# Performance work log

Measured on AMD Instinct MI355X. Metric: run time of the kernel, lower is better.

Reference implementation:

```python
import jax, jax.numpy as jnp
import numpy as np
import itertools

B, N, IN_DIM, H_DIM, OUT_DIM, K = 64, 32, 128, 512, 256, 2


def _uniform(key, shape, fan_in):
    bound = 1.0 / np.sqrt(fan_in)
    return jax.random.uniform(key, shape, jnp.float32, -bound, bound)


def setup_inputs() -> dict:
    key = jax.random.key(0)
    ks = jax.random.split(key, 7)
    x = jax.random.normal(ks[0], (B, N, IN_DIM), jnp.float32)
    W1 = _uniform(ks[1], (IN_DIM * K, H_DIM), IN_DIM * K)
    b1 = _uniform(ks[2], (H_DIM,), IN_DIM * K)
    W2 = _uniform(ks[3], (H_DIM, H_DIM), H_DIM)
    b2 = _uniform(ks[4], (H_DIM,), H_DIM)
    W3 = _uniform(ks[5], (H_DIM, OUT_DIM), H_DIM)
    b3 = _uniform(ks[6], (OUT_DIM,), H_DIM)
    return {"x": x, "W1": W1, "b1": b1, "W2": W2, "b2": b2, "W3": W3, "b3": b3}


def reference(x, W1, b1, W2, b2, W3, b3):
    n = x.shape[1]
    # all k-permutations of set indices, itertools order: [P, K], P = N*(N-1) for K=2
    perm = jnp.asarray(np.array(list(itertools.permutations(range(n), K)), dtype=np.int32))
    # gather: [B, P, K, in_dim] -> flatten last two dims -> [B, P, K*in_dim]
    xp = x[:, perm, :].reshape(x.shape[0], perm.shape[0], K * x.shape[2])
    h = jax.nn.relu(jnp.einsum('bpf,fh->bph', xp, W1) + b1)
    h = jax.nn.relu(jnp.einsum('bph,hg->bpg', h, W2) + b2)
    out = jnp.einsum('bpg,go->bpo', h, W3) + b3
    return out.sum(axis=1)  # sum over permutations -> [B, out_dim]
```

## Files before the change

### kernel.cpp

```cpp
#include <hip/hip_runtime.h>

#define BB 64
#define NN 32
#define IND 128
#define HD 512
#define OD 256
#define NPERM 992

typedef __attribute__((ext_vector_type(8))) _Float16 half8;
typedef __attribute__((ext_vector_type(4))) _Float16 half4;
typedef __attribute__((ext_vector_type(16))) float f32x16;

typedef __attribute__((address_space(3))) char lds_char_t;
typedef __attribute__((address_space(1))) const char gbl_char_t;

__device__ __forceinline__ void glds16(const void* g, void* l) {
    __builtin_amdgcn_global_load_lds((gbl_char_t*)g, (lds_char_t*)l, 16, 0, 0);
}

#define WAITVM6 asm volatile("s_waitcnt vmcnt(6)" ::: "memory")
#define WAITVM2 asm volatile("s_waitcnt vmcnt(2)" ::: "memory")
#define WAITVM1 asm volatile("s_waitcnt vmcnt(1)" ::: "memory")
#define WAITLGKM asm volatile("s_waitcnt lgkmcnt(0)" ::: "memory")
#define RBAR __builtin_amdgcn_s_barrier()

__device__ __forceinline__ half8 relu8(half8 x) {
    half8 z = 0;
    return __builtin_elementwise_max(x, z);
}

#define XTO 69632
__global__ __launch_bounds__(512, 4) void kprep(
    const float* __restrict__ x, const float* __restrict__ W1, const float* __restrict__ b1,
    const float* __restrict__ W2, _Float16* __restrict__ W2t,
    const float* __restrict__ b3, float* __restrict__ out,
    _Float16* __restrict__ U, _Float16* __restrict__ Vo) {
    __shared__ char smem[(256 + 32) * 272];
    const int bid = blockIdx.x;
    const int t = threadIdx.x;

    if (bid >= 256) {
        const int bid2 = bid - 256;
        float (*tile)[65] = (float (*)[65])smem;
        if (t < 256) out[(size_t)bid2 * OD + t] = (float)NPERM * b3[t];
        const int k0 = (bid2 & 7) * 64, c0 = (bid2 >> 3) * 64;
        const int cin = t & 63, r0 = (t >> 6) * 8;
#pragma unroll
        for (int rr = 0; rr < 8; ++rr)
            tile[r0 + rr][cin] = W2[(size_t)(k0 + r0 + rr) * HD + c0 + cin];
        __syncthreads();
        const int kout = t & 63;
#pragma unroll
        for (int rr = 0; rr < 8; ++rr) {
            int c = r0 + rr;
            W2t[(size_t)(c0 + c) * HD + k0 + kout] = (_Float16)tile[kout][c];
        }
        return;
    }

    const int g = bid & 3, b = bid >> 2;
    const int h0 = (g & 1) * 256;
    const int koff = (g >> 1) * 128;

    {
        const int n = t >> 4, c8 = (t & 15) * 8;
        const float* src = x + ((size_t)(b * NN + n)) * IND + c8;
        float4 f0 = *(const float4*)src;
        float4 f1 = *(const float4*)(src + 4);
        half8 h;
        h[0] = (_Float16)f0.x; h[1] = (_Float16)f0.y;
        h[2] = (_Float16)f0.z; h[3] = (_Float16)f0.w;
        h[4] = (_Float16)f1.x; h[5] = (_Float16)f1.y;
        h[6] = (_Float16)f1.z; h[7] = (_Float16)f1.w;
        *(half8*)(smem + XTO + n * 272 + c8 * 2) = h;
    }
    {
        const int ht = t & 63, ktb = t >> 6;
#pragma unroll
        for (int it = 0; it < 4; ++it) {
            const int kt = ktb + it * 8;
            const float* wsrc = W1 + (size_t)(koff + kt * 4) * HD + h0 + ht * 4;
            float4 v0 = *(const float4*)(wsrc);
            float4 v1 = *(const float4*)(wsrc + HD);
            float4 v2 = *(const float4*)(wsrc + 2 * HD);
            float4 v3 = *(const float4*)(wsrc + 3 * HD);
            char* wdst = smem + (size_t)(ht * 4) * 272 + kt * 8;
            half4 o0 = {(_Float16)v0.x, (_Float16)v1.x, (_Float16)v2.x, (_Float16)v3.x};
            half4 o1 = {(_Float16)v0.y, (_Float16)v1.y, (_Float16)v2.y, (_Float16)v3.y};
            half4 o2 = {(_Float16)v0.z, (_Float16)v1.z, (_Float16)v2.z, (_Float16)v3.z};
            half4 o3 = {(_Float16)v0.w, (_Float16)v1.w, (_Float16)v2.w, (_Float16)v3.w};
            *(half4*)(wdst) = o0;
            *(half4*)(wdst + 272) = o1;
            *(half4*)(wdst + 544) = o2;
            *(half4*)(wdst + 816) = o3;
        }
    }
    __syncthreads();

    const int lane = t & 63, wv = t >> 6;
    const int l31 = lane & 31, hi = lane >> 5;
    const char* abase = smem + XTO + (size_t)l31 * 272 + hi * 16;
    const char* bbase = smem + (size_t)(wv * 32 + l31) * 272 + hi * 16;

    f32x16 acc;
#pragma unroll
    for (int r = 0; r < 16; ++r) acc[r] = 0.f;
#pragma unroll
    for (int ks = 0; ks < 8; ++ks) {
        half8 a  = *(const half8*)(abase + ks * 32);
        half8 bf = *(const half8*)(bbase + ks * 32);
        acc = __builtin_amdgcn_mfma_f32_32x32x16_f16(a, bf, acc, 0, 0, 0);
    }
    const int hglob = h0 + wv * 32 + l31;
    const float bias = (g < 2) ? b1[hglob] : 0.f;
    _Float16* dst = ((g < 2) ? U : Vo) + (size_t)b * NN * HD + hglob;
#pragma unroll
    for (int r = 0; r < 16; ++r) {
        int row = (r & 3) + 8 * (r >> 2) + 4 * hi;
        dst[(size_t)row * HD] = (_Float16)(acc[r] + bias);
    }
}

#define SLOT0 65536
#define SLOT1 81920
__global__ __launch_bounds__(512, 2) void k2(
    const _Float16* __restrict__ Ug, const _Float16* __restrict__ Vg,
    const _Float16* __restrict__ W2t, const float* __restrict__ b2,
    const float* __restrict__ W3, float* __restrict__ out) {
    __shared__ char smb[98304];
    __shared__ float red[8][64];
    __shared__ float hred[64];

    const int bp = blockIdx.x;
    const int cb0 = blockIdx.y * 64;
    const int t = threadIdx.x;
    const int lane = t & 63, wid = t >> 6;
    const int l31 = lane & 31, hi = lane >> 5;
    const int lh = lane >> 5, lm = lane & 31;
    const unsigned sw = (unsigned)((l31 & 15) << 4);

    auto issueB = [&](int kh) {
#pragma unroll
        for (int ii = 0; ii < 4; ++ii) {
            int r = wid * 8 + ii * 2 + lh;
            const char* src = (const char*)W2t + (size_t)(cb0 + r) * 1024 + kh * 512
                              + ((lm * 16) ^ ((r & 15) << 4));
            glds16(src, smb + kh * 32768 + (wid * 8 + ii * 2) * 512);
        }
    };
    auto issueV = [&](int bb, int kh, unsigned slotOff) {
#pragma unroll
        for (int ii = 0; ii < 2; ++ii) {
            int r = wid * 4 + ii * 2 + lh;
            const char* src = (const char*)Vg + (size_t)(bb * NN + r) * 1024 + kh * 512
                              + ((lm * 16) ^ ((r & 15) << 4));
            glds16(src, smb + slotOff + (wid * 4 + ii * 2) * 512);
        }
    };

    const int bA = bp * 2, bB = bp * 2 + 1;
    issueB(0);
    issueV(bA, 0, SLOT0);
    issueB(1);
    issueV(bA, 1, SLOT1);
    WAITVM6;
    RBAR;

    f32x16 acc[4][2];
    auto resetAcc = [&]() {
#pragma unroll
        for (int rf = 0; rf < 4; ++rf)
#pragma unroll
            for (int cf = 0; cf < 2; ++cf)
#pragma unroll
                for (int r = 0; r < 16; ++r) acc[rf][cf][r] = 0.f;
    };

    auto compute = [&](int bb, int kh, unsigned slotOff) {
        const char* ubase = (const char*)Ug + (size_t)(bb * NN + wid * 4) * 1024
                            + kh * 512 + hi * 16;
        const unsigned vb = slotOff + (unsigned)(l31 * 512);
        const unsigned bb0 = (unsigned)(kh * 32768 + l31 * 512);
        const unsigned bb1 = (unsigned)(kh * 32768 + (32 + l31) * 512);

        half8 pU0, pU1, pU2, pU3, pV, pB0, pB1;
        {
            unsigned kx = ((unsigned)(hi * 16)) ^ sw;
            pU0 = *(const half8*)(ubase + 0 * 1024);
            pU1 = *(const half8*)(ubase + 1 * 1024);
            pU2 = *(const half8*)(ubase + 2 * 1024);
            pU3 = *(const half8*)(ubase + 3 * 1024);
            pV  = *(const half8*)(smb + vb + kx);
            pB0 = *(const half8*)(smb + bb0 + kx);
            pB1 = *(const half8*)(smb + bb1 + kx);
        }
#pragma unroll
        for (int kk = 0; kk < 16; ++kk) {
            half8 cU0 = pU0, cU1 = pU1, cU2 = pU2, cU3 = pU3;
            half8 cV = pV, cB0 = pB0, cB1 = pB1;
            if (kk < 15) {
                int kn = kk + 1;
                unsigned kx = ((unsigned)(kn * 32 + hi * 16)) ^ sw;
                pU0 = *(const half8*)(ubase + 0 * 1024 + kn * 32);
                pU1 = *(const half8*)(ubase + 1 * 1024 + kn * 32);
                pU2 = *(const half8*)(ubase + 2 * 1024 + kn * 32);
                pU3 = *(const half8*)(ubase + 3 * 1024 + kn * 32);
                pV  = *(const half8*)(smb + vb + kx);
                pB0 = *(const half8*)(smb + bb0 + kx);
                pB1 = *(const half8*)(smb + bb1 + kx);
            }

            __builtin_amdgcn_s_setprio(1);
            half8 af0 = relu8(cU0 + cV);
            acc[0][0] = __builtin_amdgcn_mfma_f32_32x32x16_f16(af0, cB0, acc[0][0], 0, 0, 0);
            acc[0][1] = __builtin_amdgcn_mfma_f32_32x32x16_f16(af0, cB1, acc[0][1], 0, 0, 0);
            half8 af1 = relu8(cU1 + cV);
            acc[1][0] = __builtin_amdgcn_mfma_f32_32x32x16_f16(af1, cB0, acc[1][0], 0, 0, 0);
            acc[1][1] = __builtin_amdgcn_mfma_f32_32x32x16_f16(af1, cB1, acc[1][1], 0, 0, 0);
            half8 af2 = relu8(cU2 + cV);
            acc[2][0] = __builtin_amdgcn_mfma_f32_32x32x16_f16(af2, cB0, acc[2][0], 0, 0, 0);
            acc[2][1] = __builtin_amdgcn_mfma_f32_32x32x16_f16(af2, cB1, acc[2][1], 0, 0, 0);
            half8 af3 = relu8(cU3 + cV);
            acc[3][0] = __builtin_amdgcn_mfma_f32_32x32x16_f16(af3, cB0, acc[3][0], 0, 0, 0);
            acc[3][1] = __builtin_amdgcn_mfma_f32_32x32x16_f16(af3, cB1, acc[3][1], 0, 0, 0);
            __builtin_amdgcn_s_setprio(0);

#pragma unroll
            for (int gq = 0; gq < 4; ++gq) {
                __builtin_amdgcn_sched_group_barrier(0x002, 8, 0);
                __builtin_amdgcn_sched_group_barrier(0x008, 2, 0);
            }
        }
    };

    auto sums_gemv = [&]() -> float {
        float scf[2];
#pragma unroll
        for (int cf = 0; cf < 2; ++cf) {
            int col = cb0 + cf * 32 + l31;
            float b2v = b2[col];
            float s = 0.f;
#pragma unroll
            for (int rf = 0; rf < 4; ++rf) {
                int i_idx = wid * 4 + rf;
#pragma unroll
                for (int r = 0; r < 16; ++r) {
                    int row = (r & 3) + 8 * (r >> 2) + 4 * hi;
                    float h2 = fmaxf(acc[rf][cf][r] + b2v, 0.f);
                    if (row != i_idx) s += h2;
                }
            }
            s += __shfl_xor(s, 32);
            scf[cf] = s;
        }
        if (lane < 32) {
            red[wid][l31] = scf[0];
            red[wid][32 + l31] = scf[1];
        }
        WAITLGKM; RBAR;
        if (t < 64) {
            float hsum = 0.f;
#pragma unroll
            for (int w = 0; w < 8; ++w) hsum += red[w][t];
            hred[t] = hsum;
        }
        WAITLGKM; RBAR;
        int o = t & 255, gg = t >> 8;
        const float* w3p = W3 + ((size_t)(cb0 + gg * 32)) * OD + o;
        float a = 0.f;
#pragma unroll 8
        for (int j = 0; j < 32; ++j)
            a += hred[gg * 32 + j] * w3p[(size_t)j * OD];
        return a;
    };

    resetAcc();
    compute(bA, 0, SLOT0);
    RBAR;
    issueV(bB, 0, SLOT0);
    WAITVM2; RBAR;
    compute(bA, 1, SLOT1);
    RBAR;
    issueV(bB, 1, SLOT1);
    float a0 = sums_gemv();
    WAITVM2; RBAR;
    resetAcc();
    compute(bB, 0, SLOT0);
    atomicAdd(&out[(size_t)bA * OD + (t & 255)], a0);
    WAITVM1; RBAR;
    compute(bB, 1, SLOT1);
    float a1 = sums_gemv();
    atomicAdd(&out[(size_t)bB * OD + (t & 255)], a1);
}

extern "C" void kernel_launch(void* const* d_in, const int* in_sizes, int n_in,
                              void* d_out, int out_size, void* d_ws, size_t ws_size,
                              hipStream_t stream) {
    const float* x  = (const float*)d_in[0];
    const float* W1 = (const float*)d_in[1];
    const float* b1 = (const float*)d_in[2];
    const float* W2 = (const float*)d_in[3];
    const float* b2 = (const float*)d_in[4];
    const float* W3 = (const float*)d_in[5];
    const float* b3 = (const float*)d_in[6];
    float* out = (float*)d_out;

    _Float16* U   = (_Float16*)d_ws;
    _Float16* V   = U + (size_t)BB * NN * HD;
    _Float16* W2t = V + (size_t)BB * NN * HD;

    hipLaunchKernelGGL(kprep, dim3(320), dim3(512), 0, stream,
                       x, W1, b1, W2, W2t, b3, out, U, V);
    hipLaunchKernelGGL(k2, dim3(32, 8), dim3(512), 0, stream, U, V, W2t, b2, W3, out);
}
```

Baseline: 43.65 us.

## Halve k2 column tile to 32 and split grid in z for occupancy

```diff
diff --git a/kernel.cpp b/kernel.cpp
--- a/kernel.cpp
+++ b/kernel.cpp
@@ -18,9 +18,9 @@
     __builtin_amdgcn_global_load_lds((gbl_char_t*)g, (lds_char_t*)l, 16, 0, 0);
 }
 
-#define WAITVM6 asm volatile("s_waitcnt vmcnt(6)" ::: "memory")
+#define WAITVM4 asm volatile("s_waitcnt vmcnt(4)" ::: "memory")
 #define WAITVM2 asm volatile("s_waitcnt vmcnt(2)" ::: "memory")
-#define WAITVM1 asm volatile("s_waitcnt vmcnt(1)" ::: "memory")
+#define WAITVM0 asm volatile("s_waitcnt vmcnt(0)" ::: "memory")
 #define WAITLGKM asm volatile("s_waitcnt lgkmcnt(0)" ::: "memory")
 #define RBAR __builtin_amdgcn_s_barrier()
 
@@ -121,18 +121,18 @@
     }
 }
 
-#define SLOT0 65536
-#define SLOT1 81920
-__global__ __launch_bounds__(512, 2) void k2(
+#define SLOT0 32768
+#define SLOT1 49152
+__global__ __launch_bounds__(512, 4) void k2(
     const _Float16* __restrict__ Ug, const _Float16* __restrict__ Vg,
     const _Float16* __restrict__ W2t, const float* __restrict__ b2,
     const float* __restrict__ W3, float* __restrict__ out) {
-    __shared__ char smb[98304];
-    __shared__ float red[8][64];
-    __shared__ float hred[64];
+    __shared__ char smb[65536];
+    __shared__ float red[8][32];
+    __shared__ float hred[32];
 
     const int bp = blockIdx.x;
-    const int cb0 = blockIdx.y * 64;
+    const int cb0 = blockIdx.y * 64 + blockIdx.z * 32;
     const int t = threadIdx.x;
     const int lane = t & 63, wid = t >> 6;
     const int l31 = lane & 31, hi = lane >> 5;
@@ -141,11 +141,11 @@
 
     auto issueB = [&](int kh) {
 #pragma unroll
-        for (int ii = 0; ii < 4; ++ii) {
-            int r = wid * 8 + ii * 2 + lh;
+        for (int ii = 0; ii < 2; ++ii) {
+            int r = wid * 4 + ii * 2 + lh;
             const char* src = (const char*)W2t + (size_t)(cb0 + r) * 1024 + kh * 512
                               + ((lm * 16) ^ ((r & 15) << 4));
-            glds16(src, smb + kh * 32768 + (wid * 8 + ii * 2) * 512);
+            glds16(src, smb + kh * 16384 + (wid * 4 + ii * 2) * 512);
         }
     };
     auto issueV = [&](int bb, int kh, unsigned slotOff) {
@@ -163,27 +163,24 @@
     issueV(bA, 0, SLOT0);
     issueB(1);
     issueV(bA, 1, SLOT1);
-    WAITVM6;
+    WAITVM4;
     RBAR;
 
-    f32x16 acc[4][2];
+    f32x16 acc[4];
     auto resetAcc = [&]() {
 #pragma unroll
         for (int rf = 0; rf < 4; ++rf)
 #pragma unroll
-            for (int cf = 0; cf < 2; ++cf)
-#pragma unroll
-                for (int r = 0; r < 16; ++r) acc[rf][cf][r] = 0.f;
+            for (int r = 0; r < 16; ++r) acc[rf][r] = 0.f;
     };
 
     auto compute = [&](int bb, int kh, unsigned slotOff) {
         const char* ubase = (const char*)Ug + (size_t)(bb * NN + wid * 4) * 1024
                             + kh * 512 + hi * 16;
         const unsigned vb = slotOff + (unsigned)(l31 * 512);
-        const unsigned bb0 = (unsigned)(kh * 32768 + l31 * 512);
-        const unsigned bb1 = (unsigned)(kh * 32768 + (32 + l31) * 512);
-
-        half8 pU0, pU1, pU2, pU3, pV, pB0, pB1;
+        const unsigned bboff = (unsigned)(kh * 16384 + l31 * 512);
+
+        half8 pU0, pU1, pU2, pU3, pV, pB0;
         {
             unsigned kx = ((unsigned)(hi * 16)) ^ sw;
             pU0 = *(const half8*)(ubase + 0 * 1024);
@@ -191,13 +188,12 @@
             pU2 = *(const half8*)(ubase + 2 * 1024);
             pU3 = *(const half8*)(ubase + 3 * 1024);
             pV  = *(const half8*)(smb + vb + kx);
-            pB0 = *(const half8*)(smb + bb0 + kx);
-            pB1 = *(const half8*)(smb + bb1 + kx);
+            pB0 = *(const half8*)(smb + bboff + kx);
         }
 #pragma unroll
         for (int kk = 0; kk < 16; ++kk) {
             half8 cU0 = pU0, cU1 = pU1, cU2 = pU2, cU3 = pU3;
-            half8 cV = pV, cB0 = pB0, cB1 = pB1;
+            half8 cV = pV, cB0 = pB0;
             if (kk < 15) {
                 int kn = kk + 1;
                 unsigned kx = ((unsigned)(kn * 32 + hi * 16)) ^ sw;
@@ -206,59 +202,46 @@
                 pU2 = *(const half8*)(ubase + 2 * 1024 + kn * 32);
                 pU3 = *(const half8*)(ubase + 3 * 1024 + kn * 32);
                 pV  = *(const half8*)(smb + vb + kx);
-                pB0 = *(const half8*)(smb + bb0 + kx);
-                pB1 = *(const half8*)(smb + bb1 + kx);
+                pB0 = *(const half8*)(smb + bboff + kx);
             }
 
             __builtin_amdgcn_s_setprio(1);
             half8 af0 = relu8(cU0 + cV);
-            acc[0][0] = __builtin_amdgcn_mfma_f32_32x32x16_f16(af0, cB0, acc[0][0], 0, 0, 0);
-            acc[0][1] = __builtin_amdgcn_mfma_f32_32x32x16_f16(af0, cB1, acc[0][1], 0, 0, 0);
+            acc[0] = __builtin_amdgcn_mfma_f32_32x32x16_f16(af0, cB0, acc[0], 0, 0, 0);
             half8 af1 = relu8(cU1 + cV);
-            acc[1][0] = __builtin_amdgcn_mfma_f32_32x32x16_f16(af1, cB0, acc[1][0], 0, 0, 0);
-            acc[1][1] = __builtin_amdgcn_mfma_f32_32x32x16_f16(af1, cB1, acc[1][1], 0, 0, 0);
+            acc[1] = __builtin_amdgcn_mfma_f32_32x32x16_f16(af1, cB0, acc[1], 0, 0, 0);
             half8 af2 = relu8(cU2 + cV);
-            acc[2][0] = __builtin_amdgcn_mfma_f32_32x32x16_f16(af2, cB0, acc[2][0], 0, 0, 0);
-            acc[2][1] = __builtin_amdgcn_mfma_f32_32x32x16_f16(af2, cB1, acc[2][1], 0, 0, 0);
+            acc[2] = __builtin_amdgcn_mfma_f32_32x32x16_f16(af2, cB0, acc[2], 0, 0, 0);
             half8 af3 = relu8(cU3 + cV);
-            acc[3][0] = __builtin_amdgcn_mfma_f32_32x32x16_f16(af3, cB0, acc[3][0], 0, 0, 0);
-            acc[3][1] = __builtin_amdgcn_mfma_f32_32x32x16_f16(af3, cB1, acc[3][1], 0, 0, 0);
+            acc[3] = __builtin_amdgcn_mfma_f32_32x32x16_f16(af3, cB0, acc[3], 0, 0, 0);
             __builtin_amdgcn_s_setprio(0);
 
 #pragma unroll
             for (int gq = 0; gq < 4; ++gq) {
                 __builtin_amdgcn_sched_group_barrier(0x002, 8, 0);
-                __builtin_amdgcn_sched_group_barrier(0x008, 2, 0);
+                __builtin_amdgcn_sched_group_barrier(0x008, 1, 0);
             }
         }
     };
 
     auto sums_gemv = [&]() -> float {
-        float scf[2];
-#pragma unroll
-        for (int cf = 0; cf < 2; ++cf) {
-            int col = cb0 + cf * 32 + l31;
-            float b2v = b2[col];
-            float s = 0.f;
-#pragma unroll
-            for (int rf = 0; rf < 4; ++rf) {
-                int i_idx = wid * 4 + rf;
-#pragma unroll
-                for (int r = 0; r < 16; ++r) {
-                    int row = (r & 3) + 8 * (r >> 2) + 4 * hi;
-                    float h2 = fmaxf(acc[rf][cf][r] + b2v, 0.f);
-                    if (row != i_idx) s += h2;
-                }
+        int col = cb0 + l31;
+        float b2v = b2[col];
+        float s = 0.f;
+#pragma unroll
+        for (int rf = 0; rf < 4; ++rf) {
+            int i_idx = wid * 4 + rf;
+#pragma unroll
+            for (int r = 0; r < 16; ++r) {
+                int row = (r & 3) + 8 * (r >> 2) + 4 * hi;
+                float h2 = fmaxf(acc[rf][r] + b2v, 0.f);
+                if (row != i_idx) s += h2;
             }
-            s += __shfl_xor(s, 32);
-            scf[cf] = s;
-        }
-        if (lane < 32) {
-            red[wid][l31] = scf[0];
-            red[wid][32 + l31] = scf[1];
-        }
+        }
+        s += __shfl_xor(s, 32);
+        if (lane < 32) red[wid][l31] = s;
         WAITLGKM; RBAR;
-        if (t < 64) {
+        if (t < 32) {
             float hsum = 0.f;
 #pragma unroll
             for (int w = 0; w < 8; ++w) hsum += red[w][t];
@@ -266,11 +249,11 @@
         }
         WAITLGKM; RBAR;
         int o = t & 255, gg = t >> 8;
-        const float* w3p = W3 + ((size_t)(cb0 + gg * 32)) * OD + o;
+        const float* w3p = W3 + ((size_t)(cb0 + gg * 16)) * OD + o;
         float a = 0.f;
 #pragma unroll 8
-        for (int j = 0; j < 32; ++j)
-            a += hred[gg * 32 + j] * w3p[(size_t)j * OD];
+        for (int j = 0; j < 16; ++j)
+            a += hred[gg * 16 + j] * w3p[(size_t)j * OD];
         return a;
     };
 
@@ -283,11 +266,10 @@
     RBAR;
     issueV(bB, 1, SLOT1);
     float a0 = sums_gemv();
-    WAITVM2; RBAR;
+    WAITVM0; RBAR;
     resetAcc();
     compute(bB, 0, SLOT0);
     atomicAdd(&out[(size_t)bA * OD + (t & 255)], a0);
-    WAITVM1; RBAR;
     compute(bB, 1, SLOT1);
     float a1 = sums_gemv();
     atomicAdd(&out[(size_t)bB * OD + (t & 255)], a1);
@@ -311,5 +293,5 @@
 
     hipLaunchKernelGGL(kprep, dim3(320), dim3(512), 0, stream,
                        x, W1, b1, W2, W2t, b3, out, U, V);
-    hipLaunchKernelGGL(k2, dim3(32, 8), dim3(512), 0, stream, U, V, W2t, b2, W3, out);
-}
+    hipLaunchKernelGGL(k2, dim3(32, 8, 2), dim3(512), 0, stream, U, V, W2t, b2, W3, out);
+}
```

Measured after the change: 65.43 us. 1.5x slower.
